# Performance work log

Hardware: AMD Instinct MI355X
Metric: run time of the kernel (lower is better)

## Reference

```python
import jax, jax.numpy as jnp
import numpy as np

NUM_SUBJECTS = 2048
NUM_TRIALS = 40  # -> num_paths = C(43,3) = 12341
NUM_STATES = 4


def _enumerate_paths(num_trials):
    # All monotone non-decreasing state sequences over {0,1,2,3}, same order
    # as the torch cached_property `paths`.
    paths = [[0], [1], [2], [3]]
    for _ in range(num_trials - 1):
        paths = [p + [s] for p in paths for s in range(p[-1], NUM_STATES)]
    return np.asarray(paths, dtype=np.int32)  # [P, T]


def setup_inputs() -> dict:
    key = jax.random.key(0)
    k1, k2, k3, k4 = jax.random.split(key, 4)
    return {
        "subject_responses": jax.random.randint(
            k1, (NUM_SUBJECTS, NUM_TRIALS), 0, NUM_STATES, dtype=jnp.int32),
        "paths": jnp.asarray(_enumerate_paths(NUM_TRIALS)),
        "w_strategy_success": jax.random.uniform(k2, (4, 4), dtype=jnp.float32),
        "w_state_priors": jax.random.uniform(k3, (4,), dtype=jnp.float32),
        "w_transitions": jax.random.uniform(k4, (4, 4), dtype=jnp.float32),
    }


def reference(subject_responses, paths, w_strategy_success, w_state_priors,
              w_transitions):
    # Fixed constants from the module
    strat_mask = jnp.triu(jnp.full((4, 4), -jnp.inf, dtype=jnp.float32), k=1)
    trans_mask = jnp.tril(jnp.full((4, 4), -jnp.inf, dtype=jnp.float32), k=-1)
    p_strategy_responses = jnp.array(
        [[3 / 9, 4 / 9, 1 / 9, 1 / 9],
         [0.0, 4 / 6, 1 / 6, 1 / 6],
         [0.0, 0.0, 0.5, 0.5],
         [0.0, 0.0, 0.0, 1.0]], dtype=jnp.float32)

    # Parameter transforms
    p_strategy_success = jax.nn.softmax(w_strategy_success + strat_mask, axis=-1)
    p_state_responses = p_strategy_success @ p_strategy_responses        # [4,4]
    p_state_priors = jax.nn.softmax(w_state_priors)                      # [4]
    p_transitions = jax.nn.softmax(w_transitions + trans_mask, axis=-1)  # [4,4]

    # P(path): log prior of first state + sum of log transition probs
    log_tr = jnp.log(p_transitions)
    log_p_paths = (jnp.log(p_state_priors)[paths[:, 0]]
                   + log_tr[paths[:, :-1], paths[:, 1:]].sum(-1))  # [P]
    p_paths = jnp.exp(log_p_paths)

    # P(responses | path) per subject: sum_t log p_state_responses[state_t, resp_t]
    # expressed as a dense contraction (P, T*4) x (T*4, S) for efficiency.
    log_sr = jnp.log(p_state_responses)                  # [state, response]
    paths_oh = jax.nn.one_hot(paths, NUM_STATES, dtype=log_sr.dtype)  # [P,T,4]
    resp_log = log_sr.T[subject_responses]               # [S,T,4]; [s,t,k]=log_sr[k, r_st]
    log_lik = jnp.einsum('ptk,stk->sp', paths_oh, resp_log)  # [S,P]
    likelihoods = jnp.exp(log_lik)

    # P(path | responses)
    numerator = p_paths[None, :] * likelihoods           # [S,P]
    posteriors = numerator / numerator.sum(-1, keepdims=True)
    return posteriors
```

## Files before the change

kernel.cpp:

```cpp
#include <hip/hip_runtime.h>
#include <math.h>

#define NSUB   2048
#define NTRIAL 40
#define NPATH  12341
#define PBLK   1024
#define NFULL  (NPATH / PBLK)
#define NTAIL  (NPATH - NFULL * PBLK)

__global__ __launch_bounds__(256) void path_kernel(
        const int* __restrict__ paths,
        const float* __restrict__ w_sp,
        const float* __restrict__ w_tr,
        int2* __restrict__ rec) {
    __shared__ float sprior[4];
    __shared__ float str[16];
    const int tid = threadIdx.x;

    if (tid < 4) {
        float m = fmaxf(fmaxf(w_sp[0], w_sp[1]), fmaxf(w_sp[2], w_sp[3]));
        float s = 0.f;
        for (int k = 0; k < 4; k++) s += __expf(w_sp[k] - m);
        sprior[tid] = w_sp[tid] - (__logf(s) + m);
    } else if (tid < 20) {
        int idx = tid - 4, i = idx >> 2, j = idx & 3;
        float m = -1e30f;
        for (int k = i; k < 4; k++) m = fmaxf(m, w_tr[i*4 + k]);
        float s = 0.f;
        for (int k = i; k < 4; k++) s += __expf(w_tr[i*4 + k] - m);
        str[idx] = (j >= i) ? (w_tr[i*4 + j] - (__logf(s) + m)) : 0.f;
    }
    __syncthreads();

    int p = blockIdx.x * 256 + tid;
    if (p >= NPATH) return;

    const int4* pp = (const int4*)(paths + (size_t)p * NTRIAL);
    int st[NTRIAL];
#pragma unroll
    for (int q = 0; q < NTRIAL / 4; q++) {
        int4 v = pp[q];
        st[4*q] = v.x; st[4*q+1] = v.y; st[4*q+2] = v.z; st[4*q+3] = v.w;
    }
    float lp = sprior[st[0]];
    int c0 = (st[0] == 0), c1 = (st[0] <= 1), c2 = (st[0] <= 2);
#pragma unroll
    for (int t = 1; t < NTRIAL; t++) {
        lp += str[st[t-1]*4 + st[t]];
        c0 += (st[t] == 0); c1 += (st[t] <= 1); c2 += (st[t] <= 2);
    }
    rec[p] = make_int2(__float_as_int(lp), c0 | (c1 << 6) | (c2 << 12));
}

__global__ __launch_bounds__(1024) void post_kernel(
        const int* __restrict__ resp,
        const float* __restrict__ w_ss,
        const int2* __restrict__ rec,
        float* __restrict__ out) {
    __shared__ float lsr[16];
    __shared__ int   rs[NTRIAL];
    __shared__ float C[4][NTRIAL + 1];
    __shared__ float D1[NTRIAL + 1], D2[NTRIAL + 1], D3[NTRIAL + 1];
    __shared__ float red[16];
    __shared__ float s_inv;

    const int s = blockIdx.x;
    const int tid = threadIdx.x;

    if (tid < 16) {
        const float psr[4][4] = {
            {3.f/9.f, 4.f/9.f, 1.f/9.f, 1.f/9.f},
            {0.f,     4.f/6.f, 1.f/6.f, 1.f/6.f},
            {0.f,     0.f,     0.5f,    0.5f},
            {0.f,     0.f,     0.f,     1.f}};
        int i = tid >> 2, r = tid & 3;
        float m = -1e30f;
        for (int j = 0; j <= i; j++) m = fmaxf(m, w_ss[i*4 + j]);
        float e[4] = {0.f,0.f,0.f,0.f}, ssum = 0.f;
        for (int j = 0; j <= i; j++) { e[j] = __expf(w_ss[i*4 + j] - m); ssum += e[j]; }
        float acc = 0.f;
        for (int j = 0; j <= i; j++) acc += (e[j] / ssum) * psr[j][r];
        lsr[tid] = __logf(acc);
    }
    if (tid < NTRIAL) rs[tid] = resp[(size_t)s * NTRIAL + tid];
    __syncthreads();

    if (tid < 4) {
        float c = 0.f;
        C[tid][0] = 0.f;
        for (int t = 0; t < NTRIAL; t++) {
            c += lsr[tid*4 + rs[t]];
            C[tid][t+1] = c;
        }
    }
    __syncthreads();
    if (tid <= NTRIAL) {
        float ct3 = C[3][NTRIAL];
        D1[tid] = C[0][tid] - C[1][tid];
        D2[tid] = C[1][tid] - C[2][tid];
        D3[tid] = C[2][tid] - C[3][tid] + ct3;
    }
    __syncthreads();

    int2 r[NFULL];
#pragma unroll
    for (int i = 0; i < NFULL; i++) r[i] = rec[tid + PBLK * i];
    const bool tail = (tid < NTAIL);
    int2 rt = tail ? rec[NFULL * PBLK + tid] : make_int2(0, 0);

    float nums[NFULL];
    float lsum = 0.f;
#pragma unroll
    for (int i = 0; i < NFULL; i++) {
        int b = r[i].y;
        int t1 = b & 63, t2 = (b >> 6) & 63, t3 = (b >> 12) & 63;
        float v = __expf(__int_as_float(r[i].x) + D1[t1] + D2[t2] + D3[t3]);
        nums[i] = v;
        lsum += v;
    }
    float numt = 0.f;
    if (tail) {
        int b = rt.y;
        int t1 = b & 63, t2 = (b >> 6) & 63, t3 = (b >> 12) & 63;
        numt = __expf(__int_as_float(rt.x) + D1[t1] + D2[t2] + D3[t3]);
        lsum += numt;
    }

    for (int off = 32; off > 0; off >>= 1)
        lsum += __shfl_down(lsum, off, 64);
    const int wave = tid >> 6, lane = tid & 63;
    if (lane == 0) red[wave] = lsum;
    __syncthreads();
    if (tid == 0) {
        float t = 0.f;
        for (int w = 0; w < 16; w++) t += red[w];
        s_inv = 1.f / t;
    }
    __syncthreads();
    const float inv = s_inv;

    float* orow = out + (size_t)s * NPATH;
#pragma unroll
    for (int i = 0; i < NFULL; i++)
        orow[tid + PBLK * i] = nums[i] * inv;
    if (tail)
        orow[NFULL * PBLK + tid] = numt * inv;
}

extern "C" void kernel_launch(void* const* d_in, const int* in_sizes, int n_in,
                              void* d_out, int out_size, void* d_ws, size_t ws_size,
                              hipStream_t stream) {
    const int*   resp  = (const int*)d_in[0];
    const int*   paths = (const int*)d_in[1];
    const float* w_ss  = (const float*)d_in[2];
    const float* w_sp  = (const float*)d_in[3];
    const float* w_tr  = (const float*)d_in[4];
    float* out = (float*)d_out;

    int2* rec = (int2*)d_ws;

    path_kernel<<<(NPATH + 255) / 256, 256, 0, stream>>>(paths, w_sp, w_tr, rec);
    post_kernel<<<NSUB, PBLK, 0, stream>>>(resp, w_ss, rec, out);
}
```

Baseline: 137.3 us.

## Use base-2 exp/log, parallel prefix scan, nontemporal stores, smaller path blocks

Scales the log-probabilities by log2(e) so the per-element exponential becomes a single native exp2 instruction, and computes the log table with the native log2 builtin. The serial 4-thread cumulative sums over trials are replaced by three wave-parallel shuffle prefix scans, and one barrier is removed. The final block reduction also uses shuffles instead of a serial loop. Output rows are written with nontemporal stores to avoid polluting cache. The path kernel drops to 64-thread blocks to spread its work over more compute units. The output write bandwidth is the dominant cost and stays unchanged.

After: 136.9 us. Within noise of the previous version (-0.3%).

```diff
diff --git a/kernel.cpp b/kernel.cpp
--- a/kernel.cpp
+++ b/kernel.cpp
@@ -8,7 +8,9 @@
 #define NFULL  (NPATH / PBLK)
 #define NTAIL  (NPATH - NFULL * PBLK)
 
-__global__ __launch_bounds__(256) void path_kernel(
+#define LOG2E  1.44269504088896340736f
+
+__global__ __launch_bounds__(64) void path_kernel(
         const int* __restrict__ paths,
         const float* __restrict__ w_sp,
         const float* __restrict__ w_tr,
@@ -21,18 +23,18 @@
         float m = fmaxf(fmaxf(w_sp[0], w_sp[1]), fmaxf(w_sp[2], w_sp[3]));
         float s = 0.f;
         for (int k = 0; k < 4; k++) s += __expf(w_sp[k] - m);
-        sprior[tid] = w_sp[tid] - (__logf(s) + m);
+        sprior[tid] = (w_sp[tid] - (__logf(s) + m)) * LOG2E;
     } else if (tid < 20) {
         int idx = tid - 4, i = idx >> 2, j = idx & 3;
         float m = -1e30f;
         for (int k = i; k < 4; k++) m = fmaxf(m, w_tr[i*4 + k]);
         float s = 0.f;
         for (int k = i; k < 4; k++) s += __expf(w_tr[i*4 + k] - m);
-        str[idx] = (j >= i) ? (w_tr[i*4 + j] - (__logf(s) + m)) : 0.f;
+        str[idx] = (j >= i) ? (w_tr[i*4 + j] - (__logf(s) + m)) * LOG2E : 0.f;
     }
     __syncthreads();
 
-    int p = blockIdx.x * 256 + tid;
+    int p = blockIdx.x * 64 + tid;
     if (p >= NPATH) return;
 
     const int4* pp = (const int4*)(paths + (size_t)p * NTRIAL);
@@ -59,14 +61,16 @@
         float* __restrict__ out) {
     __shared__ float lsr[16];
     __shared__ int   rs[NTRIAL];
-    __shared__ float C[4][NTRIAL + 1];
     __shared__ float D1[NTRIAL + 1], D2[NTRIAL + 1], D3[NTRIAL + 1];
     __shared__ float red[16];
     __shared__ float s_inv;
 
     const int s = blockIdx.x;
     const int tid = threadIdx.x;
+    const int lane = tid & 63, wave = tid >> 6;
 
+    if (wave == 3 && lane < NTRIAL)
+        rs[lane] = resp[(size_t)s * NTRIAL + lane];
     if (tid < 16) {
         const float psr[4][4] = {
             {3.f/9.f, 4.f/9.f, 1.f/9.f, 1.f/9.f},
@@ -80,25 +84,24 @@
         for (int j = 0; j <= i; j++) { e[j] = __expf(w_ss[i*4 + j] - m); ssum += e[j]; }
         float acc = 0.f;
         for (int j = 0; j <= i; j++) acc += (e[j] / ssum) * psr[j][r];
-        lsr[tid] = __logf(acc);
+        lsr[tid] = __builtin_amdgcn_logf(acc);
     }
-    if (tid < NTRIAL) rs[tid] = resp[(size_t)s * NTRIAL + tid];
     __syncthreads();
 
-    if (tid < 4) {
-        float c = 0.f;
-        C[tid][0] = 0.f;
-        for (int t = 0; t < NTRIAL; t++) {
-            c += lsr[tid*4 + rs[t]];
-            C[tid][t+1] = c;
+    if (wave < 3) {
+        float x = 0.f;
+        if (lane < NTRIAL) {
+            int rv = rs[lane];
+            x = lsr[wave*4 + rv] - lsr[wave*4 + 4 + rv];
         }
-    }
-    __syncthreads();
-    if (tid <= NTRIAL) {
-        float ct3 = C[3][NTRIAL];
-        D1[tid] = C[0][tid] - C[1][tid];
-        D2[tid] = C[1][tid] - C[2][tid];
-        D3[tid] = C[2][tid] - C[3][tid] + ct3;
+#pragma unroll
+        for (int off = 1; off < 64; off <<= 1) {
+            float y = __shfl_up(x, off, 64);
+            if (lane >= off) x += y;
+        }
+        float* D = (wave == 0) ? D1 : (wave == 1) ? D2 : D3;
+        if (lane < NTRIAL) D[lane + 1] = x;
+        if (lane == 0)     D[0] = 0.f;
     }
     __syncthreads();
 
@@ -114,7 +117,8 @@
     for (int i = 0; i < NFULL; i++) {
         int b = r[i].y;
         int t1 = b & 63, t2 = (b >> 6) & 63, t3 = (b >> 12) & 63;
-        float v = __expf(__int_as_float(r[i].x) + D1[t1] + D2[t2] + D3[t3]);
+        float v = __builtin_amdgcn_exp2f(
+            __int_as_float(r[i].x) + D1[t1] + D2[t2] + D3[t3]);
         nums[i] = v;
         lsum += v;
     }
@@ -122,19 +126,22 @@
     if (tail) {
         int b = rt.y;
         int t1 = b & 63, t2 = (b >> 6) & 63, t3 = (b >> 12) & 63;
-        numt = __expf(__int_as_float(rt.x) + D1[t1] + D2[t2] + D3[t3]);
+        numt = __builtin_amdgcn_exp2f(
+            __int_as_float(rt.x) + D1[t1] + D2[t2] + D3[t3]);
         lsum += numt;
     }
 
+#pragma unroll
     for (int off = 32; off > 0; off >>= 1)
         lsum += __shfl_down(lsum, off, 64);
-    const int wave = tid >> 6, lane = tid & 63;
     if (lane == 0) red[wave] = lsum;
     __syncthreads();
-    if (tid == 0) {
-        float t = 0.f;
-        for (int w = 0; w < 16; w++) t += red[w];
-        s_inv = 1.f / t;
+    if (tid < 64) {
+        float t = (lane < 16) ? red[lane] : 0.f;
+#pragma unroll
+        for (int off = 8; off > 0; off >>= 1)
+            t += __shfl_down(t, off, 64);
+        if (lane == 0) s_inv = 1.f / t;
     }
     __syncthreads();
     const float inv = s_inv;
@@ -142,9 +149,9 @@
     float* orow = out + (size_t)s * NPATH;
 #pragma unroll
     for (int i = 0; i < NFULL; i++)
-        orow[tid + PBLK * i] = nums[i] * inv;
+        __builtin_nontemporal_store(nums[i] * inv, &orow[tid + PBLK * i]);
     if (tail)
-        orow[NFULL * PBLK + tid] = numt * inv;
+        __builtin_nontemporal_store(numt * inv, &orow[NFULL * PBLK + tid]);
 }
 
 extern "C" void kernel_launch(void* const* d_in, const int* in_sizes, int n_in,
@@ -159,6 +166,6 @@
 
     int2* rec = (int2*)d_ws;
 
-    path_kernel<<<(NPATH + 255) / 256, 256, 0, stream>>>(paths, w_sp, w_tr, rec);
+    path_kernel<<<(NPATH + 63) / 64, 64, 0, stream>>>(paths, w_sp, w_tr, rec);
     post_kernel<<<NSUB, PBLK, 0, stream>>>(resp, w_ss, rec, out);
 }
```
